# Kernel optimization log

Hardware: AMD Instinct MI355X
Metric: run time of the kernel (lower is better)

Reference implementation:

```python
import jax, jax.numpy as jnp
import numpy as np

N_NODES = 100000
N_EDGES = 1600000
IN_CH = 64
HID = 64
OUT = 2


def sage_conv(x, src, dst, W_agg, W_root, b):
    # PyG SAGEConv (mean aggr): out = lin_l(mean_{j in N(i)} x_j) + lin_r(x_i)
    n = x.shape[0]
    msgs = x[src]                                        # [E, F] gather
    agg = jax.ops.segment_sum(msgs, dst, num_segments=n)  # [N, F] scatter-add
    cnt = jax.ops.segment_sum(jnp.ones((src.shape[0], 1), x.dtype), dst, num_segments=n)
    agg = agg / jnp.maximum(cnt, 1)                      # mean; isolated nodes -> 0
    return agg @ W_agg + x @ W_root + b


def setup_inputs() -> dict:
    key = jax.random.key(0)
    ks = jax.random.split(key, 8)
    s = lambda f: 1.0 / np.sqrt(f)
    x = jax.random.normal(ks[0], (N_NODES, IN_CH), dtype=jnp.float32)
    edge_index = jax.random.randint(ks[1], (2, N_EDGES), 0, N_NODES, dtype=jnp.int64)
    return {
        "x": x,
        "edge_index": edge_index,
        "W1_agg": jax.random.normal(ks[2], (IN_CH, HID), dtype=jnp.float32) * s(IN_CH),
        "W1_root": jax.random.normal(ks[3], (IN_CH, HID), dtype=jnp.float32) * s(IN_CH),
        "b1": jnp.zeros((HID,), jnp.float32),
        "W2_agg": jax.random.normal(ks[4], (HID, HID), dtype=jnp.float32) * s(HID),
        "W2_root": jax.random.normal(ks[5], (HID, HID), dtype=jnp.float32) * s(HID),
        "b2": jnp.zeros((HID,), jnp.float32),
        "W_lin": jax.random.normal(ks[6], (HID, OUT), dtype=jnp.float32) * s(HID),
        "b_lin": jnp.zeros((OUT,), jnp.float32),
    }


def reference(x, edge_index, W1_agg, W1_root, b1, W2_agg, W2_root, b2, W_lin, b_lin):
    src, dst = edge_index[0], edge_index[1]
    h = jax.nn.relu(sage_conv(x, src, dst, W1_agg, W1_root, b1))   # dropout = identity (eval)
    h = jax.nn.relu(sage_conv(h, src, dst, W2_agg, W2_root, b2))
    return h @ W_lin + b_lin
```

## Files before the change

### kernel.cpp

```cpp
#include <hip/hip_runtime.h>
#include <hip/hip_bf16.h>

#define FEAT 64
#define CHUNK 8192
#define MAX_NB 1024

typedef __attribute__((ext_vector_type(8))) short bf16x8;
typedef __attribute__((ext_vector_type(4))) float f32x4;

__device__ __forceinline__ float bflo2f(unsigned int u) {
    union { unsigned int u; float f; } v; v.u = u << 16; return v.f;
}
__device__ __forceinline__ float bfhi2f(unsigned int u) {
    union { unsigned int u; float f; } v; v.u = u & 0xffff0000u; return v.f;
}
__device__ __forceinline__ unsigned short f2bf(float f) {
    union { float f; unsigned int u; } v; v.f = f;
    unsigned int u = v.u;
    u += 0x7fffu + ((u >> 16) & 1u);
    return (unsigned short)(u >> 16);
}

__global__ void detect_kernel(const unsigned short* __restrict__ xh,
                              const int* __restrict__ ei32,
                              int* __restrict__ flags) {
    __shared__ int cnt_bf, cnt_nz;
    int tid = threadIdx.x;
    if (tid == 0) { cnt_bf = 0; cnt_nz = 0; }
    __syncthreads();
    unsigned short h = xh[tid * 2];
    int e = (h >> 7) & 0xFF;
    if (e >= 110 && e <= 132) atomicAdd(&cnt_bf, 1);
    if (ei32[tid * 2 + 1] != 0) atomicAdd(&cnt_nz, 1);
    __syncthreads();
    if (tid == 0) {
        flags[0] = (cnt_bf >= 128) ? 1 : 0;
        flags[1] = (cnt_nz < 8) ? 1 : 0;
    }
}

__global__ void cvt_x_kernel(const void* __restrict__ in, unsigned short* __restrict__ out16,
                             int n8, const int* __restrict__ flags) {
    if (flags[0]) return;
    int i = blockIdx.x * 256 + threadIdx.x;
    if (i >= n8) return;
    float4 a = ((const float4*)in)[2 * i];
    float4 b = ((const float4*)in)[2 * i + 1];
    uint4 o;
    o.x = (unsigned int)f2bf(a.x) | ((unsigned int)f2bf(a.y) << 16);
    o.y = (unsigned int)f2bf(a.z) | ((unsigned int)f2bf(a.w) << 16);
    o.z = (unsigned int)f2bf(b.x) | ((unsigned int)f2bf(b.y) << 16);
    o.w = (unsigned int)f2bf(b.z) | ((unsigned int)f2bf(b.w) << 16);
    ((uint4*)out16)[i] = o;
}

__global__ void cvt_weights_kernel(const void* __restrict__ w1a, const void* __restrict__ w1r,
                                   const void* __restrict__ b1,  const void* __restrict__ w2a,
                                   const void* __restrict__ w2r, const void* __restrict__ b2,
                                   const void* __restrict__ wl,  const void* __restrict__ bl,
                                   float* __restrict__ out, unsigned short* __restrict__ Wt,
                                   const int* __restrict__ flags) {
    int i = blockIdx.x * 256 + threadIdx.x;
    if (i >= 16642) return;
    const void* src; int off;
    if      (i < 4096)  { src = w1a; off = i; }
    else if (i < 8192)  { src = w1r; off = i - 4096; }
    else if (i < 8256)  { src = b1;  off = i - 8192; }
    else if (i < 12352) { src = w2a; off = i - 8256; }
    else if (i < 16448) { src = w2r; off = i - 12352; }
    else if (i < 16512) { src = b2;  off = i - 16448; }
    else if (i < 16640) { src = wl;  off = i - 16512; }
    else                { src = bl;  off = i - 16640; }
    float v = flags[0] ? bflo2f(((const unsigned short*)src)[off])
                       : ((const float*)src)[off];
    out[i] = v;
    unsigned short hv = f2bf(v);
    if (i < 4096)                      Wt[(off & 63) * 128 + (off >> 6)] = hv;
    else if (i < 8192)                 Wt[(off & 63) * 128 + 64 + (off >> 6)] = hv;
    else if (i >= 8256 && i < 12352)   Wt[8192 + (off & 63) * 128 + (off >> 6)] = hv;
    else if (i >= 12352 && i < 16448)  Wt[8192 + (off & 63) * 128 + 64 + (off >> 6)] = hv;
}

__global__ __launch_bounds__(256) void p1_hist_kernel(
    const int* __restrict__ ei32, int* __restrict__ hist,
    int E, int N, int NB, int EC, const int* __restrict__ flags) {
    __shared__ int lh[MAX_NB];
    int tid = threadIdx.x, c = blockIdx.x;
    for (int i = tid; i < NB; i += 256) lh[i] = 0;
    __syncthreads();
    int idx64 = flags[1];
    long base = (long)c * CHUNK;
#pragma unroll 4
    for (int j = 0; j < CHUNK / 256; ++j) {
        long e = base + j * 256 + tid;
        if (e < E) {
            int d = idx64 ? ei32[2 * ((long)E + e)] : ei32[(long)E + e];
            if ((unsigned)d < (unsigned)N)
                atomicAdd(&lh[d >> 8], 1);
        }
    }
    __syncthreads();
    for (int k = tid; k < NB; k += 256) hist[(long)k * EC + c] = lh[k];
}

__global__ __launch_bounds__(256) void scan1_kernel(const int* __restrict__ in,
                                                    int* __restrict__ out,
                                                    int* __restrict__ blocksum, int n) {
    int tid = threadIdx.x;
    int base = blockIdx.x * 2048 + tid * 8;
    int v[8];
    int tsum = 0;
#pragma unroll
    for (int i = 0; i < 8; ++i) {
        v[i] = (base + i < n) ? in[base + i] : 0;
        tsum += v[i];
    }
    int lane = tid & 63;
    int x = tsum;
#pragma unroll
    for (int off = 1; off < 64; off <<= 1) {
        int y = __shfl_up(x, off);
        if (lane >= off) x += y;
    }
    __shared__ int wsum[4];
    int wave = tid >> 6;
    if (lane == 63) wsum[wave] = x;
    __syncthreads();
    int woff = 0;
#pragma unroll
    for (int w = 0; w < 4; ++w) if (w < wave) woff += wsum[w];
    int run = woff + x - tsum;
#pragma unroll
    for (int i = 0; i < 8; ++i) {
        if (base + i < n) out[base + i] = run;
        run += v[i];
    }
    if (tid == 255) blocksum[blockIdx.x] = woff + x;
}

__global__ void scan3_kernel(int* __restrict__ out, const int* __restrict__ blocksum, int n) {
    int i = blockIdx.x * 256 + threadIdx.x;
    if (i >= n) return;
    int nb = i >> 11;
    int pre = 0;
    for (int b = 0; b < nb; ++b) pre += blocksum[b];
    out[i] += pre;
}

__global__ __launch_bounds__(256) void p3_scatter_kernel(
    const int* __restrict__ ei32, const int* __restrict__ hscan,
    int* __restrict__ bkt, int E, int N, int NB, int EC,
    const int* __restrict__ flags) {
    __shared__ int lh[MAX_NB];
    int tid = threadIdx.x, c = blockIdx.x;
    for (int i = tid; i < NB; i += 256) lh[i] = 0;
    __syncthreads();
    int idx64 = flags[1];
    long base = (long)c * CHUNK;
#pragma unroll 4
    for (int j = 0; j < CHUNK / 256; ++j) {
        long e = base + j * 256 + tid;
        if (e < E) {
            int s = idx64 ? ei32[2 * e]             : ei32[e];
            int d = idx64 ? ei32[2 * ((long)E + e)] : ei32[(long)E + e];
            if ((unsigned)d < (unsigned)N) {
                if ((unsigned)s >= (unsigned)N) s = 0;
                int k = d >> 8;
                int r = atomicAdd(&lh[k], 1);
                bkt[hscan[(long)k * EC + c] + r] = s | ((d & 255) << 20);
            }
        }
    }
}

__global__ __launch_bounds__(256) void p4_build_kernel(
    const int* __restrict__ bkt, const int* __restrict__ hscan, const int* __restrict__ hist,
    int* __restrict__ offs, int* __restrict__ cnt, int* __restrict__ srcs,
    int E, int N, int NB, int EC) {
    int k = blockIdx.x, tid = threadIdx.x;
    int start = hscan[(long)k * EC];
    int end = (k + 1 < NB) ? hscan[(long)(k + 1) * EC]
                           : (hscan[(long)NB * EC - 1] + hist[(long)NB * EC - 1]);
    __shared__ int lc[256], lheads[256], wsum[4];
    lc[tid] = 0;
    __syncthreads();
    for (int e = start + tid; e < end; e += 256)
        atomicAdd(&lc[(bkt[e] >> 20) & 255], 1);
    __syncthreads();
    int cv = lc[tid];
    int lane = tid & 63, wave = tid >> 6;
    int x = cv;
#pragma unroll
    for (int off = 1; off < 64; off <<= 1) {
        int y = __shfl_up(x, off);
        if (lane >= off) x += y;
    }
    if (lane == 63) wsum[wave] = x;
    __syncthreads();
    int woff = 0;
#pragma unroll
    for (int w = 0; w < 4; ++w) if (w < wave) woff += wsum[w];
    int excl = woff + x - cv;
    int gnode = k * 256 + tid;
    if (gnode < N) { offs[gnode] = start + excl; cnt[gnode] = cv; }
    lheads[tid] = excl;
    __syncthreads();
    for (int e = start + tid; e < end; e += 256) {
        int p = bkt[e];
        int d8 = (p >> 20) & 255;
        int pos = start + atomicAdd(&lheads[d8], 1);
        srcs[pos] = p & 0xFFFFF;
    }
}

__global__ __launch_bounds__(256) void aggregate_kernel(
    const void* __restrict__ feat_raw, const unsigned short* __restrict__ feat_ws,
    const int* __restrict__ srcs,
    const int* __restrict__ offs, const int* __restrict__ cnt,
    unsigned short* __restrict__ agg16, int N, const int* __restrict__ flags) {
    const unsigned short* feat16 = flags[0] ? (const unsigned short*)feat_raw : feat_ws;
    long gid = (long)blockIdx.x * 256 + threadIdx.x;
    int node = (int)(gid >> 6);
    if (node >= N) return;
    int lane = threadIdx.x & 63;
    int g = lane >> 3;
    int li = lane & 7;
    int start = offs[node];
    int deg = cnt[node];
    int end = start + deg;
    float acc[8] = {0.f, 0.f, 0.f, 0.f, 0.f, 0.f, 0.f, 0.f};
    int e = start;
    for (; e + 16 <= end; e += 16) {
        int s0 = srcs[e + g];
        int s1 = srcs[e + 8 + g];
        uint4 u0 = *(const uint4*)(feat16 + (size_t)s0 * FEAT + 8 * li);
        uint4 u1 = *(const uint4*)(feat16 + (size_t)s1 * FEAT + 8 * li);
        acc[0] += bflo2f(u0.x & 0xffffu); acc[1] += bfhi2f(u0.x);
        acc[2] += bflo2f(u0.y & 0xffffu); acc[3] += bfhi2f(u0.y);
        acc[4] += bflo2f(u0.z & 0xffffu); acc[5] += bfhi2f(u0.z);
        acc[6] += bflo2f(u0.w & 0xffffu); acc[7] += bfhi2f(u0.w);
        acc[0] += bflo2f(u1.x & 0xffffu); acc[1] += bfhi2f(u1.x);
        acc[2] += bflo2f(u1.y & 0xffffu); acc[3] += bfhi2f(u1.y);
        acc[4] += bflo2f(u1.z & 0xffffu); acc[5] += bfhi2f(u1.z);
        acc[6] += bflo2f(u1.w & 0xffffu); acc[7] += bfhi2f(u1.w);
    }
    for (; e < end; e += 8) {
        int idx = e + g;
        bool ok = idx < end;
        int s = srcs[ok ? idx : end - 1];
        uint4 u = *(const uint4*)(feat16 + (size_t)s * FEAT + 8 * li);
        if (ok) {
            acc[0] += bflo2f(u.x & 0xffffu); acc[1] += bfhi2f(u.x);
            acc[2] += bflo2f(u.y & 0xffffu); acc[3] += bfhi2f(u.y);
            acc[4] += bflo2f(u.z & 0xffffu); acc[5] += bfhi2f(u.z);
            acc[6] += bflo2f(u.w & 0xffffu); acc[7] += bfhi2f(u.w);
        }
    }
#pragma unroll
    for (int i = 0; i < 8; ++i) {
        acc[i] += __shfl_xor(acc[i], 8);
        acc[i] += __shfl_xor(acc[i], 16);
        acc[i] += __shfl_xor(acc[i], 32);
    }
    if (g == 0) {
        float inv = 1.0f / (float)(deg > 0 ? deg : 1);
        uint4 o;
        o.x = (unsigned)f2bf(acc[0] * inv) | ((unsigned)f2bf(acc[1] * inv) << 16);
        o.y = (unsigned)f2bf(acc[2] * inv) | ((unsigned)f2bf(acc[3] * inv) << 16);
        o.z = (unsigned)f2bf(acc[4] * inv) | ((unsigned)f2bf(acc[5] * inv) << 16);
        o.w = (unsigned)f2bf(acc[6] * inv) | ((unsigned)f2bf(acc[7] * inv) << 16);
        *(uint4*)(agg16 + (size_t)node * FEAT + 8 * li) = o;
    }
}

__global__ __launch_bounds__(256) void sage_gemm_kernel(
    const unsigned short* __restrict__ agg16,
    const void* __restrict__ root_raw, const unsigned short* __restrict__ root_ws,
    const unsigned short* __restrict__ Wt, const float* __restrict__ bias,
    unsigned short* __restrict__ out16, int N,
    const float* __restrict__ wl, const float* __restrict__ bl,
    void* __restrict__ out_final, const int* __restrict__ flags, int root_sel) {

    const unsigned short* root16 =
        (root_sel && !flags[0]) ? root_ws : (const unsigned short*)root_raw;

    __shared__ unsigned short A_l[64][136];
    __shared__ unsigned short B_l[64][136];

    int tid = threadIdx.x;
    int blk = blockIdx.x;

#pragma unroll
    for (int i = 0; i < 4; ++i) {
        int ch = tid + i * 256;
        int n = ch >> 4, kc = ch & 15;
        *(uint4*)&B_l[n][kc * 8] = *(const uint4*)(Wt + n * 128 + kc * 8);
    }
#pragma unroll
    for (int i = 0; i < 4; ++i) {
        int ch = tid + i * 256;
        int r = ch >> 4, c = ch & 15;
        int row = blk * 64 + r;
        uint4 u = make_uint4(0, 0, 0, 0);
        if (row < N)
            u = (c < 8) ? ((const uint4*)(agg16 + (size_t)row * FEAT))[c]
                        : ((const uint4*)(root16 + (size_t)row * FEAT))[c - 8];
        *(uint4*)&A_l[r][c * 8] = u;
    }
    __syncthreads();

    int lane = tid & 63;
    int wave = tid >> 6;
    int r0 = wave * 16;
    int m = lane & 15, quad = lane >> 4;

    f32x4 acc0 = {0.f, 0.f, 0.f, 0.f};
    f32x4 acc1 = acc0, acc2 = acc0, acc3 = acc0;

#pragma unroll
    for (int k0 = 0; k0 < 128; k0 += 32) {
        bf16x8 a = *(const bf16x8*)&A_l[r0 + m][k0 + quad * 8];
        bf16x8 b0 = *(const bf16x8*)&B_l[ 0 + m][k0 + quad * 8];
        bf16x8 b1 = *(const bf16x8*)&B_l[16 + m][k0 + quad * 8];
        bf16x8 b2 = *(const bf16x8*)&B_l[32 + m][k0 + quad * 8];
        bf16x8 b3 = *(const bf16x8*)&B_l[48 + m][k0 + quad * 8];
        acc0 = __builtin_amdgcn_mfma_f32_16x16x32_bf16(a, b0, acc0, 0, 0, 0);
        acc1 = __builtin_amdgcn_mfma_f32_16x16x32_bf16(a, b1, acc1, 0, 0, 0);
        acc2 = __builtin_amdgcn_mfma_f32_16x16x32_bf16(a, b2, acc2, 0, 0, 0);
        acc3 = __builtin_amdgcn_mfma_f32_16x16x32_bf16(a, b3, acc3, 0, 0, 0);
    }
    __syncthreads();

#pragma unroll
    for (int c = 0; c < 4; ++c) {
        f32x4 av = (c == 0) ? acc0 : (c == 1) ? acc1 : (c == 2) ? acc2 : acc3;
        float bv = bias[c * 16 + m];
#pragma unroll
        for (int reg = 0; reg < 4; ++reg) {
            float v = fmaxf(av[reg] + bv, 0.f);
            A_l[r0 + quad * 4 + reg][c * 16 + m] = f2bf(v);
        }
    }
    __syncthreads();

#pragma unroll
    for (int i = 0; i < 2; ++i) {
        int ch = tid + i * 256;
        int r = ch >> 3, c = ch & 7;
        int row = blk * 64 + r;
        if (row < N)
            ((uint4*)(out16 + (size_t)row * FEAT))[c] = *(const uint4*)&A_l[r][c * 8];
    }

    if (wl) {
        int r = tid >> 2, part = tid & 3;
        int row = blk * 64 + r;
        if (row < N) {
            float p0 = 0.f, p1 = 0.f;
#pragma unroll
            for (int j = 0; j < 16; ++j) {
                int f = part * 16 + j;
                float v = bflo2f(A_l[r][f]);
                p0 += v * wl[f * 2 + 0];
                p1 += v * wl[f * 2 + 1];
            }
            p0 += __shfl_down(p0, 2, 4); p0 += __shfl_down(p0, 1, 4);
            p1 += __shfl_down(p1, 2, 4); p1 += __shfl_down(p1, 1, 4);
            if (part == 0) {
                p0 += bl[0];
                p1 += bl[1];
                if (flags[0]) {
                    unsigned int o = ((unsigned int)f2bf(p1) << 16) | (unsigned int)f2bf(p0);
                    ((unsigned int*)out_final)[row] = o;
                } else {
                    ((float2*)out_final)[row] = make_float2(p0, p1);
                }
            }
        }
    }
}

extern "C" void kernel_launch(void* const* d_in, const int* in_sizes, int n_in,
                              void* d_out, int out_size, void* d_ws, size_t ws_size,
                              hipStream_t stream) {
    const void* x_in = d_in[0];
    const int*  ei32 = (const int*)d_in[1];

    int N = in_sizes[0] / FEAT;
    int E = in_sizes[1] / 2;
    int NB = (N + 255) >> 8;
    int EC = (E + CHUNK - 1) / CHUNK;
    int HN = NB * EC;

    unsigned short* x16   = (unsigned short*)d_ws;
    unsigned short* h16   = x16 + (size_t)N * FEAT;
    unsigned short* agg16 = h16 + (size_t)N * FEAT;
    unsigned short* Wt    = agg16 + (size_t)N * FEAT;
    float*          wbuf  = (float*)(Wt + 16384);
    int*            hist  = (int*)(wbuf + 16704);
    int*            hscan = hist + HN;
    int*            bsum  = hscan + HN;
    int*            flags = bsum + 1024;
    int*            offs  = flags + 16;
    int*            cnt   = offs + N;
    int*            bkt   = cnt + N;
    int*            srcs  = bkt + E;

    float* b1_32 = wbuf + 8192;
    float* b2_32 = wbuf + 16448;
    float* wl32  = wbuf + 16512;
    float* bl32  = wbuf + 16640;

    detect_kernel<<<1, 256, 0, stream>>>((const unsigned short*)x_in, ei32, flags);

    int n8 = N * FEAT / 8;
    cvt_x_kernel<<<(n8 + 255) / 256, 256, 0, stream>>>(x_in, x16, n8, flags);
    cvt_weights_kernel<<<(16642 + 255) / 256, 256, 0, stream>>>(
        d_in[2], d_in[3], d_in[4], d_in[5], d_in[6], d_in[7], d_in[8], d_in[9],
        wbuf, Wt, flags);

    p1_hist_kernel<<<EC, 256, 0, stream>>>(ei32, hist, E, N, NB, EC, flags);
    int sB = (HN + 2047) / 2048;
    scan1_kernel<<<sB, 256, 0, stream>>>(hist, hscan, bsum, HN);
    scan3_kernel<<<(HN + 255) / 256, 256, 0, stream>>>(hscan, bsum, HN);
    p3_scatter_kernel<<<EC, 256, 0, stream>>>(ei32, hscan, bkt, E, N, NB, EC, flags);
    p4_build_kernel<<<NB, 256, 0, stream>>>(bkt, hscan, hist, offs, cnt, srcs, E, N, NB, EC);

    int aBlocks = (int)(((long)N * 64 + 255) / 256);
    int gBlocks = (N + 63) / 64;

    aggregate_kernel<<<aBlocks, 256, 0, stream>>>(x_in, x16, srcs, offs, cnt, agg16, N, flags);
    sage_gemm_kernel<<<gBlocks, 256, 0, stream>>>(agg16, x_in, x16, Wt, b1_32, h16, N,
                                                  nullptr, nullptr, nullptr, flags, 1);

    aggregate_kernel<<<aBlocks, 256, 0, stream>>>(h16, h16, srcs, offs, cnt, agg16, N, flags);
    sage_gemm_kernel<<<gBlocks, 256, 0, stream>>>(agg16, h16, h16, Wt + 8192, b2_32, h16, N,
                                                  wl32, bl32, d_out, flags, 0);
}
```

Before: 261.9 us.

## Fuse neighbor aggregation into GEMM kernel and merge prep and scan launches

Moves the mean aggregation into the per-layer GEMM kernel, so each block gathers neighbor features for its 64 rows straight into shared memory and skips the agg16 round trip through global memory. Weight conversion is merged into the detect kernel, the two-pass scan becomes a single-block serial scan, and layer 2 no longer writes h16. This cuts several launches and some global traffic. The cost is lower aggregation parallelism: one block now handles 64 nodes, 16 per wave, serially instead of one wave per node. The single-block scan is also serialized.

```diff
diff --git a/kernel.cpp b/kernel.cpp
--- a/kernel.cpp
+++ b/kernel.cpp
@@ -21,9 +21,14 @@
     return (unsigned short)(u >> 16);
 }
 
-__global__ void detect_kernel(const unsigned short* __restrict__ xh,
-                              const int* __restrict__ ei32,
-                              int* __restrict__ flags) {
+__global__ __launch_bounds__(256) void prep_kernel(
+    const unsigned short* __restrict__ xh, const int* __restrict__ ei32,
+    const void* __restrict__ w1a, const void* __restrict__ w1r,
+    const void* __restrict__ b1,  const void* __restrict__ w2a,
+    const void* __restrict__ w2r, const void* __restrict__ b2,
+    const void* __restrict__ wl,  const void* __restrict__ bl,
+    float* __restrict__ wbuf, unsigned short* __restrict__ Wt,
+    int* __restrict__ flags) {
     __shared__ int cnt_bf, cnt_nz;
     int tid = threadIdx.x;
     if (tid == 0) { cnt_bf = 0; cnt_nz = 0; }
@@ -33,9 +38,29 @@
     if (e >= 110 && e <= 132) atomicAdd(&cnt_bf, 1);
     if (ei32[tid * 2 + 1] != 0) atomicAdd(&cnt_nz, 1);
     __syncthreads();
+    int f0 = (cnt_bf >= 128) ? 1 : 0;
     if (tid == 0) {
-        flags[0] = (cnt_bf >= 128) ? 1 : 0;
+        flags[0] = f0;
         flags[1] = (cnt_nz < 8) ? 1 : 0;
+    }
+    for (int i = tid; i < 16642; i += 256) {
+        const void* src; int off;
+        if      (i < 4096)  { src = w1a; off = i; }
+        else if (i < 8192)  { src = w1r; off = i - 4096; }
+        else if (i < 8256)  { src = b1;  off = i - 8192; }
+        else if (i < 12352) { src = w2a; off = i - 8256; }
+        else if (i < 16448) { src = w2r; off = i - 12352; }
+        else if (i < 16512) { src = b2;  off = i - 16448; }
+        else if (i < 16640) { src = wl;  off = i - 16512; }
+        else                { src = bl;  off = i - 16640; }
+        float v = f0 ? bflo2f(((const unsigned short*)src)[off])
+                     : ((const float*)src)[off];
+        wbuf[i] = v;
+        unsigned short hv = f2bf(v);
+        if (i < 4096)                      Wt[(off & 63) * 128 + (off >> 6)] = hv;
+        else if (i < 8192)                 Wt[(off & 63) * 128 + 64 + (off >> 6)] = hv;
+        else if (i >= 8256 && i < 12352)   Wt[8192 + (off & 63) * 128 + (off >> 6)] = hv;
+        else if (i >= 12352 && i < 16448)  Wt[8192 + (off & 63) * 128 + 64 + (off >> 6)] = hv;
     }
 }
 
@@ -54,33 +79,6 @@
     ((uint4*)out16)[i] = o;
 }
 
-__global__ void cvt_weights_kernel(const void* __restrict__ w1a, const void* __restrict__ w1r,
-                                   const void* __restrict__ b1,  const void* __restrict__ w2a,
-                                   const void* __restrict__ w2r, const void* __restrict__ b2,
-                                   const void* __restrict__ wl,  const void* __restrict__ bl,
-                                   float* __restrict__ out, unsigned short* __restrict__ Wt,
-                                   const int* __restrict__ flags) {
-    int i = blockIdx.x * 256 + threadIdx.x;
-    if (i >= 16642) return;
-    const void* src; int off;
-    if      (i < 4096)  { src = w1a; off = i; }
-    else if (i < 8192)  { src = w1r; off = i - 4096; }
-    else if (i < 8256)  { src = b1;  off = i - 8192; }
-    else if (i < 12352) { src = w2a; off = i - 8256; }
-    else if (i < 16448) { src = w2r; off = i - 12352; }
-    else if (i < 16512) { src = b2;  off = i - 16448; }
-    else if (i < 16640) { src = wl;  off = i - 16512; }
-    else                { src = bl;  off = i - 16640; }
-    float v = flags[0] ? bflo2f(((const unsigned short*)src)[off])
-                       : ((const float*)src)[off];
-    out[i] = v;
-    unsigned short hv = f2bf(v);
-    if (i < 4096)                      Wt[(off & 63) * 128 + (off >> 6)] = hv;
-    else if (i < 8192)                 Wt[(off & 63) * 128 + 64 + (off >> 6)] = hv;
-    else if (i >= 8256 && i < 12352)   Wt[8192 + (off & 63) * 128 + (off >> 6)] = hv;
-    else if (i >= 12352 && i < 16448)  Wt[8192 + (off & 63) * 128 + 64 + (off >> 6)] = hv;
-}
-
 __global__ __launch_bounds__(256) void p1_hist_kernel(
     const int* __restrict__ ei32, int* __restrict__ hist,
     int E, int N, int NB, int EC, const int* __restrict__ flags) {
@@ -103,48 +101,44 @@
     for (int k = tid; k < NB; k += 256) hist[(long)k * EC + c] = lh[k];
 }
 
-__global__ __launch_bounds__(256) void scan1_kernel(const int* __restrict__ in,
-                                                    int* __restrict__ out,
-                                                    int* __restrict__ blocksum, int n) {
-    int tid = threadIdx.x;
-    int base = blockIdx.x * 2048 + tid * 8;
-    int v[8];
-    int tsum = 0;
-#pragma unroll
-    for (int i = 0; i < 8; ++i) {
-        v[i] = (base + i < n) ? in[base + i] : 0;
-        tsum += v[i];
-    }
-    int lane = tid & 63;
-    int x = tsum;
-#pragma unroll
-    for (int off = 1; off < 64; off <<= 1) {
-        int y = __shfl_up(x, off);
-        if (lane >= off) x += y;
-    }
+__global__ __launch_bounds__(256) void scan_kernel(const int* __restrict__ in,
+                                                   int* __restrict__ out, int n) {
     __shared__ int wsum[4];
-    int wave = tid >> 6;
-    if (lane == 63) wsum[wave] = x;
-    __syncthreads();
-    int woff = 0;
-#pragma unroll
-    for (int w = 0; w < 4; ++w) if (w < wave) woff += wsum[w];
-    int run = woff + x - tsum;
-#pragma unroll
-    for (int i = 0; i < 8; ++i) {
-        if (base + i < n) out[base + i] = run;
-        run += v[i];
-    }
-    if (tid == 255) blocksum[blockIdx.x] = woff + x;
-}
-
-__global__ void scan3_kernel(int* __restrict__ out, const int* __restrict__ blocksum, int n) {
-    int i = blockIdx.x * 256 + threadIdx.x;
-    if (i >= n) return;
-    int nb = i >> 11;
-    int pre = 0;
-    for (int b = 0; b < nb; ++b) pre += blocksum[b];
-    out[i] += pre;
+    __shared__ int carry_s;
+    int tid = threadIdx.x, lane = tid & 63, wave = tid >> 6;
+    if (tid == 0) carry_s = 0;
+    __syncthreads();
+    for (int base = 0; base < n; base += 2048) {
+        int idx0 = base + tid * 8;
+        int v[8];
+        int tsum = 0;
+#pragma unroll
+        for (int i = 0; i < 8; ++i) {
+            v[i] = (idx0 + i < n) ? in[idx0 + i] : 0;
+            tsum += v[i];
+        }
+        int x = tsum;
+#pragma unroll
+        for (int off = 1; off < 64; off <<= 1) {
+            int y = __shfl_up(x, off);
+            if (lane >= off) x += y;
+        }
+        if (lane == 63) wsum[wave] = x;
+        __syncthreads();
+        int woff = 0;
+#pragma unroll
+        for (int w = 0; w < 4; ++w) if (w < wave) woff += wsum[w];
+        int total = wsum[0] + wsum[1] + wsum[2] + wsum[3];
+        int mycarry = carry_s;
+        int run = mycarry + woff + x - tsum;
+#pragma unroll
+        for (int i = 0; i < 8; ++i) {
+            if (idx0 + i < n) out[idx0 + i] = run;
+            run += v[i];
+        }
+        __syncthreads();
+        if (tid == 0) carry_s = mycarry + total;
+    }
 }
 
 __global__ __launch_bounds__(256) void p3_scatter_kernel(
@@ -213,76 +207,16 @@
     }
 }
 
-__global__ __launch_bounds__(256) void aggregate_kernel(
-    const void* __restrict__ feat_raw, const unsigned short* __restrict__ feat_ws,
-    const int* __restrict__ srcs,
-    const int* __restrict__ offs, const int* __restrict__ cnt,
-    unsigned short* __restrict__ agg16, int N, const int* __restrict__ flags) {
-    const unsigned short* feat16 = flags[0] ? (const unsigned short*)feat_raw : feat_ws;
-    long gid = (long)blockIdx.x * 256 + threadIdx.x;
-    int node = (int)(gid >> 6);
-    if (node >= N) return;
-    int lane = threadIdx.x & 63;
-    int g = lane >> 3;
-    int li = lane & 7;
-    int start = offs[node];
-    int deg = cnt[node];
-    int end = start + deg;
-    float acc[8] = {0.f, 0.f, 0.f, 0.f, 0.f, 0.f, 0.f, 0.f};
-    int e = start;
-    for (; e + 16 <= end; e += 16) {
-        int s0 = srcs[e + g];
-        int s1 = srcs[e + 8 + g];
-        uint4 u0 = *(const uint4*)(feat16 + (size_t)s0 * FEAT + 8 * li);
-        uint4 u1 = *(const uint4*)(feat16 + (size_t)s1 * FEAT + 8 * li);
-        acc[0] += bflo2f(u0.x & 0xffffu); acc[1] += bfhi2f(u0.x);
-        acc[2] += bflo2f(u0.y & 0xffffu); acc[3] += bfhi2f(u0.y);
-        acc[4] += bflo2f(u0.z & 0xffffu); acc[5] += bfhi2f(u0.z);
-        acc[6] += bflo2f(u0.w & 0xffffu); acc[7] += bfhi2f(u0.w);
-        acc[0] += bflo2f(u1.x & 0xffffu); acc[1] += bfhi2f(u1.x);
-        acc[2] += bflo2f(u1.y & 0xffffu); acc[3] += bfhi2f(u1.y);
-        acc[4] += bflo2f(u1.z & 0xffffu); acc[5] += bfhi2f(u1.z);
-        acc[6] += bflo2f(u1.w & 0xffffu); acc[7] += bfhi2f(u1.w);
-    }
-    for (; e < end; e += 8) {
-        int idx = e + g;
-        bool ok = idx < end;
-        int s = srcs[ok ? idx : end - 1];
-        uint4 u = *(const uint4*)(feat16 + (size_t)s * FEAT + 8 * li);
-        if (ok) {
-            acc[0] += bflo2f(u.x & 0xffffu); acc[1] += bfhi2f(u.x);
-            acc[2] += bflo2f(u.y & 0xffffu); acc[3] += bfhi2f(u.y);
-            acc[4] += bflo2f(u.z & 0xffffu); acc[5] += bfhi2f(u.z);
-            acc[6] += bflo2f(u.w & 0xffffu); acc[7] += bfhi2f(u.w);
-        }
-    }
-#pragma unroll
-    for (int i = 0; i < 8; ++i) {
-        acc[i] += __shfl_xor(acc[i], 8);
-        acc[i] += __shfl_xor(acc[i], 16);
-        acc[i] += __shfl_xor(acc[i], 32);
-    }
-    if (g == 0) {
-        float inv = 1.0f / (float)(deg > 0 ? deg : 1);
-        uint4 o;
-        o.x = (unsigned)f2bf(acc[0] * inv) | ((unsigned)f2bf(acc[1] * inv) << 16);
-        o.y = (unsigned)f2bf(acc[2] * inv) | ((unsigned)f2bf(acc[3] * inv) << 16);
-        o.z = (unsigned)f2bf(acc[4] * inv) | ((unsigned)f2bf(acc[5] * inv) << 16);
-        o.w = (unsigned)f2bf(acc[6] * inv) | ((unsigned)f2bf(acc[7] * inv) << 16);
-        *(uint4*)(agg16 + (size_t)node * FEAT + 8 * li) = o;
-    }
-}
-
-__global__ __launch_bounds__(256) void sage_gemm_kernel(
-    const unsigned short* __restrict__ agg16,
-    const void* __restrict__ root_raw, const unsigned short* __restrict__ root_ws,
+__global__ __launch_bounds__(256) void fused_layer_kernel(
+    const void* __restrict__ gsrc_raw, const unsigned short* __restrict__ gsrc_ws,
+    const int* __restrict__ srcs, const int* __restrict__ offs, const int* __restrict__ cnt,
     const unsigned short* __restrict__ Wt, const float* __restrict__ bias,
     unsigned short* __restrict__ out16, int N,
     const float* __restrict__ wl, const float* __restrict__ bl,
-    void* __restrict__ out_final, const int* __restrict__ flags, int root_sel) {
-
-    const unsigned short* root16 =
-        (root_sel && !flags[0]) ? root_ws : (const unsigned short*)root_raw;
+    void* __restrict__ out_final, const int* __restrict__ flags, int sel) {
+
+    const unsigned short* feat16 =
+        (sel && !flags[0]) ? gsrc_ws : (const unsigned short*)gsrc_raw;
 
     __shared__ unsigned short A_l[64][136];
     __shared__ unsigned short B_l[64][136];
@@ -297,20 +231,72 @@
         *(uint4*)&B_l[n][kc * 8] = *(const uint4*)(Wt + n * 128 + kc * 8);
     }
 #pragma unroll
-    for (int i = 0; i < 4; ++i) {
+    for (int i = 0; i < 2; ++i) {
         int ch = tid + i * 256;
-        int r = ch >> 4, c = ch & 15;
+        int r = ch >> 3, c = ch & 7;
         int row = blk * 64 + r;
         uint4 u = make_uint4(0, 0, 0, 0);
-        if (row < N)
-            u = (c < 8) ? ((const uint4*)(agg16 + (size_t)row * FEAT))[c]
-                        : ((const uint4*)(root16 + (size_t)row * FEAT))[c - 8];
-        *(uint4*)&A_l[r][c * 8] = u;
-    }
-    __syncthreads();
+        if (row < N) u = ((const uint4*)(feat16 + (size_t)row * FEAT))[c];
+        *(uint4*)&A_l[r][64 + c * 8] = u;
+    }
 
     int lane = tid & 63;
     int wave = tid >> 6;
+    int g = lane >> 3;
+    int li = lane & 7;
+    for (int i = 0; i < 16; ++i) {
+        int r = wave * 16 + i;
+        int node = blk * 64 + r;
+        if (node >= N) break;
+        int start = offs[node];
+        int deg = cnt[node];
+        int end = start + deg;
+        float acc[8] = {0.f, 0.f, 0.f, 0.f, 0.f, 0.f, 0.f, 0.f};
+        int e = start;
+        for (; e + 16 <= end; e += 16) {
+            int s0 = srcs[e + g];
+            int s1 = srcs[e + 8 + g];
+            uint4 u0 = *(const uint4*)(feat16 + (size_t)s0 * FEAT + 8 * li);
+            uint4 u1 = *(const uint4*)(feat16 + (size_t)s1 * FEAT + 8 * li);
+            acc[0] += bflo2f(u0.x & 0xffffu); acc[1] += bfhi2f(u0.x);
+            acc[2] += bflo2f(u0.y & 0xffffu); acc[3] += bfhi2f(u0.y);
+            acc[4] += bflo2f(u0.z & 0xffffu); acc[5] += bfhi2f(u0.z);
+            acc[6] += bflo2f(u0.w & 0xffffu); acc[7] += bfhi2f(u0.w);
+            acc[0] += bflo2f(u1.x & 0xffffu); acc[1] += bfhi2f(u1.x);
+            acc[2] += bflo2f(u1.y & 0xffffu); acc[3] += bfhi2f(u1.y);
+            acc[4] += bflo2f(u1.z & 0xffffu); acc[5] += bfhi2f(u1.z);
+            acc[6] += bflo2f(u1.w & 0xffffu); acc[7] += bfhi2f(u1.w);
+        }
+        for (; e < end; e += 8) {
+            int idx = e + g;
+            bool ok = idx < end;
+            int s = srcs[ok ? idx : end - 1];
+            uint4 u = *(const uint4*)(feat16 + (size_t)s * FEAT + 8 * li);
+            if (ok) {
+                acc[0] += bflo2f(u.x & 0xffffu); acc[1] += bfhi2f(u.x);
+                acc[2] += bflo2f(u.y & 0xffffu); acc[3] += bfhi2f(u.y);
+                acc[4] += bflo2f(u.z & 0xffffu); acc[5] += bfhi2f(u.z);
+                acc[6] += bflo2f(u.w & 0xffffu); acc[7] += bfhi2f(u.w);
+            }
+        }
+#pragma unroll
+        for (int j = 0; j < 8; ++j) {
+            acc[j] += __shfl_xor(acc[j], 8);
+            acc[j] += __shfl_xor(acc[j], 16);
+            acc[j] += __shfl_xor(acc[j], 32);
+        }
+        if (g == 0) {
+            float inv = 1.0f / (float)(deg > 0 ? deg : 1);
+            uint4 o;
+            o.x = (unsigned)f2bf(acc[0] * inv) | ((unsigned)f2bf(acc[1] * inv) << 16);
+            o.y = (unsigned)f2bf(acc[2] * inv) | ((unsigned)f2bf(acc[3] * inv) << 16);
+            o.z = (unsigned)f2bf(acc[4] * inv) | ((unsigned)f2bf(acc[5] * inv) << 16);
+            o.w = (unsigned)f2bf(acc[6] * inv) | ((unsigned)f2bf(acc[7] * inv) << 16);
+            *(uint4*)&A_l[r][li * 8] = o;
+        }
+    }
+    __syncthreads();
+
     int r0 = wave * 16;
     int m = lane & 15, quad = lane >> 4;
 
@@ -343,13 +329,15 @@
     }
     __syncthreads();
 
-#pragma unroll
-    for (int i = 0; i < 2; ++i) {
-        int ch = tid + i * 256;
-        int r = ch >> 3, c = ch & 7;
-        int row = blk * 64 + r;
-        if (row < N)
-            ((uint4*)(out16 + (size_t)row * FEAT))[c] = *(const uint4*)&A_l[r][c * 8];
+    if (out16) {
+#pragma unroll
+        for (int i = 0; i < 2; ++i) {
+            int ch = tid + i * 256;
+            int r = ch >> 3, c = ch & 7;
+            int row = blk * 64 + r;
+            if (row < N)
+                ((uint4*)(out16 + (size_t)row * FEAT))[c] = *(const uint4*)&A_l[r][c * 8];
+        }
     }
 
     if (wl) {
@@ -394,13 +382,11 @@
 
     unsigned short* x16   = (unsigned short*)d_ws;
     unsigned short* h16   = x16 + (size_t)N * FEAT;
-    unsigned short* agg16 = h16 + (size_t)N * FEAT;
-    unsigned short* Wt    = agg16 + (size_t)N * FEAT;
+    unsigned short* Wt    = h16 + (size_t)N * FEAT;
     float*          wbuf  = (float*)(Wt + 16384);
     int*            hist  = (int*)(wbuf + 16704);
     int*            hscan = hist + HN;
-    int*            bsum  = hscan + HN;
-    int*            flags = bsum + 1024;
+    int*            flags = hscan + HN;
     int*            offs  = flags + 16;
     int*            cnt   = offs + N;
     int*            bkt   = cnt + N;
@@ -411,29 +397,26 @@
     float* wl32  = wbuf + 16512;
     float* bl32  = wbuf + 16640;
 
-    detect_kernel<<<1, 256, 0, stream>>>((const unsigned short*)x_in, ei32, flags);
+    prep_kernel<<<1, 256, 0, stream>>>((const unsigned short*)x_in, ei32,
+                                       d_in[2], d_in[3], d_in[4], d_in[5],
+                                       d_in[6], d_in[7], d_in[8], d_in[9],
+                                       wbuf, Wt, flags);
 
     int n8 = N * FEAT / 8;
     cvt_x_kernel<<<(n8 + 255) / 256, 256, 0, stream>>>(x_in, x16, n8, flags);
-    cvt_weights_kernel<<<(16642 + 255) / 256, 256, 0, stream>>>(
-        d_in[2], d_in[3], d_in[4], d_in[5], d_in[6], d_in[7], d_in[8], d_in[9],
-        wbuf, Wt, flags);
 
     p1_hist_kernel<<<EC, 256, 0, stream>>>(ei32, hist, E, N, NB, EC, flags);
-    int sB = (HN + 2047) / 2048;
-    scan1_kernel<<<sB, 256, 0, stream>>>(hist, hscan, bsum, HN);
-    scan3_kernel<<<(HN + 255) / 256, 256, 0, stream>>>(hscan, bsum, HN);
+    scan_kernel<<<1, 256, 0, stream>>>(hist, hscan, HN);
     p3_scatter_kernel<<<EC, 256, 0, stream>>>(ei32, hscan, bkt, E, N, NB, EC, flags);
     p4_build_kernel<<<NB, 256, 0, stream>>>(bkt, hscan, hist, offs, cnt, srcs, E, N, NB, EC);
 
-    int aBlocks = (int)(((long)N * 64 + 255) / 256);
     int gBlocks = (N + 63) / 64;
 
-    aggregate_kernel<<<aBlocks, 256, 0, stream>>>(x_in, x16, srcs, offs, cnt, agg16, N, flags);
-    sage_gemm_kernel<<<gBlocks, 256, 0, stream>>>(agg16, x_in, x16, Wt, b1_32, h16, N,
-                                                  nullptr, nullptr, nullptr, flags, 1);
-
-    aggregate_kernel<<<aBlocks, 256, 0, stream>>>(h16, h16, srcs, offs, cnt, agg16, N, flags);
-    sage_gemm_kernel<<<gBlocks, 256, 0, stream>>>(agg16, h16, h16, Wt + 8192, b2_32, h16, N,
-                                                  wl32, bl32, d_out, flags, 0);
-}
+    fused_layer_kernel<<<gBlocks, 256, 0, stream>>>(
+        x_in, x16, srcs, offs, cnt, Wt, b1_32, h16, N,
+        nullptr, nullptr, nullptr, flags, 1);
+
+    fused_layer_kernel<<<gBlocks, 256, 0, stream>>>(
+        h16, h16, srcs, offs, cnt, Wt + 8192, b2_32, nullptr, N,
+        wl32, bl32, d_out, flags, 0);
+}
```

After: 414.2 us. +58.2%, slower.
